# Optimization experiments

Hardware: AMD Instinct MI355X
Metric: run time of the kernel (lower is better)

The kernel has to match this reference:

```python
import jax, jax.numpy as jnp
import numpy as np

NUM_HEADS = 16
D_MODEL = 1024
D_K = D_MODEL // NUM_HEADS
MAX_SEQ_LEN = 4096
ROPE_BASE = 10000.0
BATCH = 2
SEQ_LEN = 2048


def _rope_tables(seq_len, d_k, base=ROPE_BASE):
    # theta_i = 1 / base^(2i/d_k), i = 0..d_k/2-1
    theta = 1.0 / base ** (jnp.arange(0, d_k, 2, dtype=jnp.float32) / d_k)
    m = jnp.arange(seq_len, dtype=jnp.float32)
    m_theta = jnp.outer(m, theta)                      # [S, d_k/2]
    ang = jnp.concatenate([m_theta, m_theta], axis=-1)  # [S, d_k]
    return jnp.cos(ang), jnp.sin(ang)


def _apply_rope(x, cos, sin):
    # x: [B, H, S, d_k]; rotate-half: cat(-x2, x1)
    d2 = x.shape[-1] // 2
    x1, x2 = x[..., :d2], x[..., d2:]
    x_flip = jnp.concatenate([-x2, x1], axis=-1)
    return x * cos + x_flip * sin


def setup_inputs() -> dict:
    key = jax.random.key(0)
    kx, kq, kk, kv, ko = jax.random.split(key, 5)
    s = 1.0 / np.sqrt(D_MODEL)  # ~ nn.Linear default init scale
    x = jax.random.normal(kx, (BATCH, SEQ_LEN, D_MODEL), dtype=jnp.float32)
    W_Q = jax.random.uniform(kq, (D_MODEL, D_MODEL), jnp.float32, -s, s)
    W_K = jax.random.uniform(kk, (D_MODEL, D_MODEL), jnp.float32, -s, s)
    W_V = jax.random.uniform(kv, (D_MODEL, D_MODEL), jnp.float32, -s, s)
    W_O = jax.random.uniform(ko, (D_MODEL, D_MODEL), jnp.float32, -s, s)
    return {"x": x, "W_Q": W_Q, "W_K": W_K, "W_V": W_V, "W_O": W_O}


def reference(x, W_Q, W_K, W_V, W_O):
    B, S, _ = x.shape
    # Linear with weight [out, in]: y = x @ W.T
    def proj(W):
        y = jnp.einsum('bsd,ed->bse', x, W)
        return y.reshape(B, S, NUM_HEADS, D_K).transpose(0, 2, 1, 3)  # [B,H,S,dk]
    Q, K, V = proj(W_Q), proj(W_K), proj(W_V)
    cos, sin = _rope_tables(S, D_K)
    Q = _apply_rope(Q, cos, sin)
    K = _apply_rope(K, cos, sin)
    scores = jnp.einsum('bhsd,bhtd->bhst', Q, K) / jnp.sqrt(jnp.float32(D_K))
    causal = jnp.tril(jnp.ones((S, S), dtype=bool))
    scores = jnp.where(causal[None, None], scores, -jnp.inf)
    attn = jax.nn.softmax(scores, axis=-1)
    out = jnp.einsum('bhst,bhtd->bhsd', attn, V)
    out = out.transpose(0, 2, 1, 3).reshape(B, S, D_MODEL)
    return jnp.einsum('bsd,ed->bse', out, W_O)
```

## Files before the change

kernel.cpp:

```cpp
#include <hip/hip_runtime.h>
#include <hip/hip_bf16.h>

#define BATCH 2
#define SEQ 2048
#define DM 1024
#define NH 16
#define DKH 64

typedef __attribute__((ext_vector_type(8))) __bf16 bf16x8;
typedef __attribute__((ext_vector_type(4))) float f32x4;
typedef __attribute__((ext_vector_type(2))) float f32x2;
typedef __attribute__((ext_vector_type(8))) unsigned short ushort8;

__device__ __forceinline__ void gload16(const void* g, void* l) {
  __builtin_amdgcn_global_load_lds(
      (const __attribute__((address_space(1))) void*)g,
      (__attribute__((address_space(3))) void*)l, 16, 0, 0);
}

__global__ void cast_x(const float* __restrict__ in, __bf16* __restrict__ out) {
  int i = blockIdx.x * blockDim.x + threadIdx.x;
  f32x4 a = ((const f32x4*)in)[2 * i], b = ((const f32x4*)in)[2 * i + 1];
  bf16x8 o;
  o[0]=(__bf16)a[0]; o[1]=(__bf16)a[1]; o[2]=(__bf16)a[2]; o[3]=(__bf16)a[3];
  o[4]=(__bf16)b[0]; o[5]=(__bf16)b[1]; o[6]=(__bf16)b[2]; o[7]=(__bf16)b[3];
  ((bf16x8*)out)[i] = o;
}

__global__ void cast_w(const float* __restrict__ w0, const float* __restrict__ w1,
                       const float* __restrict__ w2, const float* __restrict__ w3,
                       __bf16* __restrict__ out) {
  const float* src = (blockIdx.y == 0) ? w0 : (blockIdx.y == 1) ? w1
                   : (blockIdx.y == 2) ? w2 : w3;
  __bf16* dst = out + (size_t)blockIdx.y * (DM * DM);
  int i = blockIdx.x * blockDim.x + threadIdx.x;
  f32x4 a = ((const f32x4*)src)[2 * i], b = ((const f32x4*)src)[2 * i + 1];
  bf16x8 o;
  o[0]=(__bf16)a[0]; o[1]=(__bf16)a[1]; o[2]=(__bf16)a[2]; o[3]=(__bf16)a[3];
  o[4]=(__bf16)b[0]; o[5]=(__bf16)b[1]; o[6]=(__bf16)b[2]; o[7]=(__bf16)b[3];
  ((bf16x8*)dst)[i] = o;
}

__global__ void gen_tab(float* __restrict__ tab) {
  int idx = blockIdx.x * blockDim.x + threadIdx.x;
  int s = idx >> 5, i = idx & 31;
  float theta = exp2f((float)i * -0.41524101186092029f);
  float sn, c;
  sincosf((float)s * theta, &sn, &c);
  tab[2 * idx] = c;
  tab[2 * idx + 1] = sn;
}

#define QSCALE 0.1803368801111137f

template<int EPI, int BN>
__launch_bounds__(256, 3)
__global__ void gemm_bt(const __bf16* __restrict__ A, const __bf16* __restrict__ B,
                        void* __restrict__ Cout, int M, int N, int K,
                        const float* __restrict__ tab) {
  __shared__ __bf16 As[128 * 64];
  __shared__ __bf16 Bs[BN * 64];
  const int tid = threadIdx.x;
  const int lane = tid & 63;
  const int w = tid >> 6;
  const int wr = w >> 1, wc = w & 1;
  const int fr = lane & 15, fq = lane >> 4;
  const int lid = blockIdx.y * gridDim.x + blockIdx.x;
  const int total = gridDim.x * gridDim.y;
  const int nlid = (lid >> 3) + (lid & 7) * (total >> 3);
  const int bx = nlid & 31;
  const int by = nlid >> 5;
  const int m0 = bx * 128;
  const int n0 = by * BN;
  const int NFR = BN / 32;

  f32x4 acc[4][BN / 32] = {};
  const int NT = K >> 6;

  for (int kt = 0; kt < NT; ++kt) {
    const int k0 = kt << 6;
    __syncthreads();
    #pragma unroll
    for (int p = 0; p < 4; ++p) {
      int c = p * 256 + tid;
      int row = c >> 3, cs = (c & 7) ^ (row & 7);
      gload16(&A[(size_t)(m0 + row) * K + k0 + cs * 8], &As[(p * 256 + w * 64) * 8]);
    }
    #pragma unroll
    for (int p = 0; p < BN / 32; ++p) {
      int c = p * 256 + tid;
      int row = c >> 3, cs = (c & 7) ^ (row & 7);
      gload16(&B[(size_t)(n0 + row) * K + k0 + cs * 8], &Bs[(p * 256 + w * 64) * 8]);
    }
    __syncthreads();
    #pragma unroll
    for (int kk = 0; kk < 2; ++kk) {
      bf16x8 af[4], bfr[BN / 32];
      #pragma unroll
      for (int mf = 0; mf < 4; ++mf) {
        int row = wr * 64 + mf * 16 + fr;
        af[mf] = *(const bf16x8*)&As[row * 64 + ((kk * 32 + fq * 8) ^ ((fr & 7) << 3))];
      }
      #pragma unroll
      for (int nf = 0; nf < NFR; ++nf) {
        int row = wc * (BN / 2) + nf * 16 + fr;
        bfr[nf] = *(const bf16x8*)&Bs[row * 64 + ((kk * 32 + fq * 8) ^ ((fr & 7) << 3))];
      }
      __builtin_amdgcn_s_setprio(1);
      #pragma unroll
      for (int mf = 0; mf < 4; ++mf)
        #pragma unroll
        for (int nf = 0; nf < NFR; ++nf)
          acc[mf][nf] = __builtin_amdgcn_mfma_f32_16x16x32_bf16(af[mf], bfr[nf], acc[mf][nf], 0, 0, 0);
      __builtin_amdgcn_s_setprio(0);
    }
  }

  if (EPI == 0) {
    const int nbase = n0 + wc * 64;
    const int which = nbase >> 10;
    const int h = (nbase & 1023) >> 6;
    const int b = m0 >> 11;
    __bf16* base0 = (__bf16*)Cout + (size_t)which * (4u << 20);
    if (which < 2) {
      const float scale = (which == 0) ? QSCALE : 1.0f;
      __bf16* dst = base0 + ((size_t)(b * NH + h)) * SEQ * DKH;
      #pragma unroll
      for (int mf = 0; mf < 4; ++mf) {
        #pragma unroll
        for (int j = 0; j < 4; ++j) {
          int s = (m0 & (SEQ - 1)) + wr * 64 + mf * 16 + fq * 4 + j;
          #pragma unroll
          for (int nf = 0; nf < 2; ++nf) {
            int i = nf * 16 + fr;
            f32x2 cs = ((const f32x2*)tab)[s * 32 + i];
            float a = acc[mf][nf][j], bb = acc[mf][nf + 2][j];
            dst[(size_t)s * DKH + i]      = (__bf16)((a * cs[0] - bb * cs[1]) * scale);
            dst[(size_t)s * DKH + i + 32] = (__bf16)((bb * cs[0] + a * cs[1]) * scale);
          }
        }
      }
    } else {
      __bf16* dst = base0 + ((size_t)(b * NH + h)) * DKH * SEQ;
      #pragma unroll
      for (int mf = 0; mf < 4; ++mf) {
        #pragma unroll
        for (int nf = 0; nf < 4; ++nf) {
          int dk = nf * 16 + fr;
          #pragma unroll
          for (int j = 0; j < 4; ++j) {
            int sp = (m0 & (SEQ - 1)) + wr * 64 + (mf >> 1) * 32 + fq * 8 + (mf & 1) * 4 + j;
            dst[(size_t)dk * SEQ + sp] = (__bf16)acc[mf][nf][j];
          }
        }
      }
    }
  } else {
    #pragma unroll
    for (int mf = 0; mf < 4; ++mf)
      #pragma unroll
      for (int nf = 0; nf < NFR; ++nf)
        #pragma unroll
        for (int j = 0; j < 4; ++j) {
          int m = m0 + wr * 64 + mf * 16 + fq * 4 + j;
          int n = n0 + wc * (BN / 2) + nf * 16 + fr;
          ((float*)Cout)[(size_t)m * N + n] = acc[mf][nf][j];
        }
  }
}

__launch_bounds__(512, 4)
__global__ void attn_causal(const __bf16* __restrict__ Qg, const __bf16* __restrict__ Kg,
                            const __bf16* __restrict__ Vtg, __bf16* __restrict__ Out,
                            float* __restrict__ P0, float* __restrict__ P1,
                            float* __restrict__ L0, float* __restrict__ L1) {
  __shared__ __bf16 Ks[2][64 * 64];
  __shared__ __bf16 Vts[2][64 * 64];
  const int tid = threadIdx.x;
  const int lane = tid & 63;
  const int w = tid >> 6;
  const int fr = lane & 15, fq = lane >> 4;
  const int bid = blockIdx.x;
  const int bh = bid >> 4;
  const int slot = bid & 15;
  const bool isA = slot < 8;
  const int qa = slot;
  const int qb = isA ? (15 - slot) : slot;
  const int sw  = isA ? (2 * qa + 2) : 99;
  const int off = isA ? (15 - 2 * qa) : 0;
  const int b = bh >> 4, h = bh & 15;
  const __bf16* Qh = Qg + (size_t)bh * SEQ * DKH;
  const __bf16* Kh = Kg + (size_t)bh * SEQ * DKH;
  const __bf16* Vth = Vtg + (size_t)bh * DKH * SEQ;

  int qrow_lo = (isA ? qa : qb) * 128 + w * 16;

  bf16x8 qf[2];
  #pragma unroll
  for (int kk = 0; kk < 2; ++kk)
    qf[kk] = *(const bf16x8*)&Qh[(size_t)(qrow_lo + fr) * DKH + kk * 32 + fq * 8];

  f32x4 Oa[4] = {};
  float lsum = 0.f;

  {
    int cch = w * 64 + lane;
    int row = cch >> 3, cs = (cch & 7) ^ (row & 7);
    gload16(&Kh[(size_t)row * DKH + cs * 8], &Ks[0][(w * 64) * 8]);
    gload16(&Vth[(size_t)row * SEQ + cs * 8], &Vts[0][(w * 64) * 8]);
  }
  __syncthreads();

  for (int it = 0; it < 17; ++it) {
    const int cur = it & 1;
    if (it + 1 < 17) {
      const int nx = it + 1;
      const int kvn = (nx < sw) ? nx : nx + off;
      const int tn = kvn << 6;
      int cch = w * 64 + lane;
      int row = cch >> 3, cs = (cch & 7) ^ (row & 7);
      gload16(&Kh[(size_t)(tn + row) * DKH + cs * 8], &Ks[cur ^ 1][(w * 64) * 8]);
      gload16(&Vth[(size_t)row * SEQ + tn + cs * 8], &Vts[cur ^ 1][(w * 64) * 8]);
    }
    if (isA && it == sw) {
      float ls = lsum;
      ls += __shfl_xor(ls, 16);
      ls += __shfl_xor(ls, 32);
      float rl[4];
      #pragma unroll
      for (int j = 0; j < 4; ++j)
        rl[j] = 1.0f / __shfl(ls, fq * 4 + j);
      #pragma unroll
      for (int nf = 0; nf < 4; ++nf)
        #pragma unroll
        for (int j = 0; j < 4; ++j) {
          int qr = qrow_lo + fq * 4 + j;
          Out[((size_t)(b * SEQ) + qr) * DM + h * DKH + nf * 16 + fr] =
              (__bf16)(Oa[nf][j] * rl[j]);
        }
      #pragma unroll
      for (int nf = 0; nf < 4; ++nf) Oa[nf] = (f32x4){0.f, 0.f, 0.f, 0.f};
      lsum = 0.f;
      qrow_lo = qb * 128 + w * 16;
      #pragma unroll
      for (int kk = 0; kk < 2; ++kk)
        qf[kk] = *(const bf16x8*)&Qh[(size_t)(qrow_lo + fr) * DKH + kk * 32 + fq * 8];
    }
    const int kvt = (it < sw) ? it : it + off;
    const int ts = kvt << 6;
    if (ts <= qrow_lo + 15) {
      f32x4 sacc[4] = {};
      __builtin_amdgcn_s_setprio(1);
      #pragma unroll
      for (int kk = 0; kk < 2; ++kk) {
        #pragma unroll
        for (int nf = 0; nf < 4; ++nf) {
          int krow = nf * 16 + fr;
          bf16x8 kf = *(const bf16x8*)&Ks[cur][krow * 64 + ((kk * 32 + fq * 8) ^ ((fr & 7) << 3))];
          sacc[nf] = __builtin_amdgcn_mfma_f32_16x16x32_bf16(kf, qf[kk], sacc[nf], 0, 0, 0);
        }
      }
      __builtin_amdgcn_s_setprio(0);
      const bool need_mask = (ts + 63 > qrow_lo);
      if (need_mask) {
        const int qr = qrow_lo + fr;
        #pragma unroll
        for (int nf = 0; nf < 4; ++nf) {
          #pragma unroll
          for (int j = 0; j < 4; ++j) {
            float v = sacc[nf][j];
            int tc = ts + nf * 16 + fq * 4 + j;
            if (tc > qr) v = -INFINITY;
            float pv = exp2f(v);
            lsum += pv;
            sacc[nf][j] = pv;
          }
        }
      } else {
        #pragma unroll
        for (int nf = 0; nf < 4; ++nf) {
          #pragma unroll
          for (int j = 0; j < 4; ++j) {
            float pv = exp2f(sacc[nf][j]);
            lsum += pv;
            sacc[nf][j] = pv;
          }
        }
      }
      bf16x8 pa[2];
      #pragma unroll
      for (int kk = 0; kk < 2; ++kk)
        #pragma unroll
        for (int e = 0; e < 8; ++e)
          pa[kk][e] = (__bf16)sacc[2 * kk + (e >> 2)][e & 3];
      __builtin_amdgcn_s_setprio(1);
      #pragma unroll
      for (int kk = 0; kk < 2; ++kk) {
        #pragma unroll
        for (int nf = 0; nf < 4; ++nf) {
          int d = nf * 16 + fr;
          bf16x8 vf = *(const bf16x8*)&Vts[cur][d * 64 + ((kk * 32 + fq * 8) ^ ((fr & 7) << 3))];
          Oa[nf] = __builtin_amdgcn_mfma_f32_16x16x32_bf16(pa[kk], vf, Oa[nf], 0, 0, 0);
        }
      }
      __builtin_amdgcn_s_setprio(0);
    }
    __syncthreads();
  }
  float* P = isA ? P1 : P0;
  float* L = isA ? L1 : L0;
  const int rbase = ((bh << 3) + (qb - 8)) << 7;
  float ls = lsum;
  ls += __shfl_xor(ls, 16);
  ls += __shfl_xor(ls, 32);
  if (lane < 16) L[rbase + w * 16 + lane] = ls;
  #pragma unroll
  for (int nf = 0; nf < 4; ++nf)
    #pragma unroll
    for (int j = 0; j < 4; ++j)
      P[(size_t)(rbase + w * 16 + fq * 4 + j) * 64 + nf * 16 + fr] = Oa[nf][j];
}

__global__ void combine(const float* __restrict__ P0, const float* __restrict__ P1,
                        const float* __restrict__ L0, const float* __restrict__ L1,
                        __bf16* __restrict__ Ab) {
  int t = blockIdx.x * blockDim.x + threadIdx.x;
  int rowid = t >> 3, d0 = (t & 7) * 8;
  int bh = rowid >> 10, rem = rowid & 1023;
  int tq = rem >> 7, r = rem & 127;
  float rl = 1.0f / (L0[rowid] + L1[rowid]);
  const float* p0 = P0 + (size_t)rowid * 64 + d0;
  const float* p1 = P1 + (size_t)rowid * 64 + d0;
  f32x4 a0 = *(const f32x4*)p0, a1 = *(const f32x4*)(p0 + 4);
  f32x4 b0 = *(const f32x4*)p1, b1 = *(const f32x4*)(p1 + 4);
  bf16x8 o;
  #pragma unroll
  for (int e = 0; e < 4; ++e) {
    o[e]     = (__bf16)((a0[e] + b0[e]) * rl);
    o[e + 4] = (__bf16)((a1[e] + b1[e]) * rl);
  }
  int s = (tq + 8) * 128 + r;
  int b = bh >> 4, h = bh & 15;
  *(bf16x8*)&Ab[((size_t)b * SEQ + s) * DM + h * DKH + d0] = o;
}

extern "C" void kernel_launch(void* const* d_in, const int* in_sizes, int n_in,
                              void* d_out, int out_size, void* d_ws, size_t ws_size,
                              hipStream_t stream) {
  const float* x  = (const float*)d_in[0];
  const float* Wq = (const float*)d_in[1];
  const float* Wk = (const float*)d_in[2];
  const float* Wv = (const float*)d_in[3];
  const float* Wo = (const float*)d_in[4];

  char* ws = (char*)d_ws;
  __bf16* xb  = (__bf16*)(ws);
  __bf16* wqb = (__bf16*)(ws + ( 8u << 20));
  __bf16* wob = (__bf16*)(ws + (14u << 20));
  __bf16* Qb  = (__bf16*)(ws + (16u << 20));
  __bf16* Kb  = (__bf16*)(ws + (24u << 20));
  __bf16* Vtb = (__bf16*)(ws + (32u << 20));
  __bf16* Ab  = (__bf16*)(ws + (40u << 20));
  float*  tab = (float*)(ws + (48u << 20));
  float*  L0  = (float*)(ws + (49u << 20));
  float*  L1  = (float*)(ws + (49u << 20) + (1u << 18));
  float* P0 = (float*)d_out;
  float* P1 = P0 + (32768 * 64);

  cast_x<<<dim3(2048), dim3(256), 0, stream>>>(x, xb);
  cast_w<<<dim3(512, 4), dim3(256), 0, stream>>>(Wq, Wk, Wv, Wo, wqb);
  gen_tab<<<dim3(256), dim3(256), 0, stream>>>(tab);

  gemm_bt<0, 128><<<dim3(32, 24), dim3(256), 0, stream>>>(xb, wqb, Qb, BATCH * SEQ, 3 * DM, DM, tab);

  attn_causal<<<dim3(512), dim3(512), 0, stream>>>(Qb, Kb, Vtb, Ab, P0, P1, L0, L1);

  combine<<<dim3(1024), dim3(256), 0, stream>>>(P0, P1, L0, L1, Ab);

  gemm_bt<1, 64><<<dim3(32, 16), dim3(256), 0, stream>>>(Ab, wob, d_out, BATCH * SEQ, DM, DM, nullptr);
}
```

Measured before the change: 104.3 us.

## Triple-buffer K/V tiles in causal attention with deeper async prefetch

Extends the K/V shared-memory ring from two to three buffers and prefetches two tiles ahead via global_load_lds. The end-of-iteration __syncthreads is replaced by an explicit vmcnt wait plus a single barrier at the start of each iteration. This is meant to hide global load latency and remove one barrier per iteration. The cost is more LDS per block, which may reduce resident blocks per CU.

```diff
diff --git a/kernel.cpp b/kernel.cpp
--- a/kernel.cpp
+++ b/kernel.cpp
@@ -174,8 +174,8 @@
                             const __bf16* __restrict__ Vtg, __bf16* __restrict__ Out,
                             float* __restrict__ P0, float* __restrict__ P1,
                             float* __restrict__ L0, float* __restrict__ L1) {
-  __shared__ __bf16 Ks[2][64 * 64];
-  __shared__ __bf16 Vts[2][64 * 64];
+  __shared__ __bf16 Ks[3][64 * 64];
+  __shared__ __bf16 Vts[3][64 * 64];
   const int tid = threadIdx.x;
   const int lane = tid & 63;
   const int w = tid >> 6;
@@ -195,6 +195,16 @@
 
   int qrow_lo = (isA ? qa : qb) * 128 + w * 16;
 
+  const int cch = w * 64 + lane;
+  const int srow = cch >> 3;
+  const int scs = ((cch & 7) ^ (srow & 7)) * 8;
+
+#define STAGE(buf, kvt) {                                                     \
+    gload16(&Kh[(size_t)(((kvt) << 6) + srow) * DKH + scs],                   \
+            &Ks[buf][(w * 64) * 8]);                                          \
+    gload16(&Vth[(size_t)srow * SEQ + ((kvt) << 6) + scs],                    \
+            &Vts[buf][(w * 64) * 8]); }
+
   bf16x8 qf[2];
   #pragma unroll
   for (int kk = 0; kk < 2; ++kk)
@@ -203,24 +213,19 @@
   f32x4 Oa[4] = {};
   float lsum = 0.f;
 
-  {
-    int cch = w * 64 + lane;
-    int row = cch >> 3, cs = (cch & 7) ^ (row & 7);
-    gload16(&Kh[(size_t)row * DKH + cs * 8], &Ks[0][(w * 64) * 8]);
-    gload16(&Vth[(size_t)row * SEQ + cs * 8], &Vts[0][(w * 64) * 8]);
-  }
-  __syncthreads();
+  STAGE(0, 0);
+  STAGE(1, 1);
 
   for (int it = 0; it < 17; ++it) {
-    const int cur = it & 1;
-    if (it + 1 < 17) {
-      const int nx = it + 1;
+    const int cur = it % 3;
+    if (it < 16) asm volatile("s_waitcnt vmcnt(2)" ::: "memory");
+    else         asm volatile("s_waitcnt vmcnt(0)" ::: "memory");
+    __builtin_amdgcn_s_barrier();
+    if (it + 2 < 17) {
+      const int nx = it + 2;
       const int kvn = (nx < sw) ? nx : nx + off;
-      const int tn = kvn << 6;
-      int cch = w * 64 + lane;
-      int row = cch >> 3, cs = (cch & 7) ^ (row & 7);
-      gload16(&Kh[(size_t)(tn + row) * DKH + cs * 8], &Ks[cur ^ 1][(w * 64) * 8]);
-      gload16(&Vth[(size_t)row * SEQ + tn + cs * 8], &Vts[cur ^ 1][(w * 64) * 8]);
+      const int nb = (it + 2) % 3;
+      STAGE(nb, kvn);
     }
     if (isA && it == sw) {
       float ls = lsum;
@@ -305,8 +310,8 @@
       }
       __builtin_amdgcn_s_setprio(0);
     }
-    __syncthreads();
   }
+#undef STAGE
   float* P = isA ? P1 : P0;
   float* L = isA ? L1 : L0;
   const int rbase = ((bh << 3) + (qb - 8)) << 7;
```

After: 103.7 us. Within noise of the previous version (-0.6%).

## Stage 128-row KV tiles per barrier and remap block order in causal attention

Applied to the files above, without the earlier changes.

The attention kernel now loads K and V^T tiles of 128 keys per double-buffer stage instead of 64. Each stage is processed as two 64-key sub-tiles, which cuts the loop from 17 iterations with barriers to at most 9. Block IDs are also remapped so that consecutive blocks are spread across head/slot groups, likely to improve load balance or cache locality across XCDs. The cost is twice the LDS per block (64KB), which may reduce occupancy under the 512x4 launch bounds, plus some wasted loads for partially masked tiles.

```diff
diff --git a/kernel.cpp b/kernel.cpp
--- a/kernel.cpp
+++ b/kernel.cpp
@@ -174,20 +174,22 @@
                             const __bf16* __restrict__ Vtg, __bf16* __restrict__ Out,
                             float* __restrict__ P0, float* __restrict__ P1,
                             float* __restrict__ L0, float* __restrict__ L1) {
-  __shared__ __bf16 Ks[2][64 * 64];
-  __shared__ __bf16 Vts[2][64 * 64];
+  __shared__ __bf16 Ks[2][128 * 64];
+  __shared__ __bf16 Vts[2][64 * 128];
   const int tid = threadIdx.x;
   const int lane = tid & 63;
   const int w = tid >> 6;
   const int fr = lane & 15, fq = lane >> 4;
-  const int bid = blockIdx.x;
-  const int bh = bid >> 4;
-  const int slot = bid & 15;
+  const int r = blockIdx.x;
+  const int nlid = (r & 7) * 64 + (r >> 3);
+  const int bh = nlid >> 4;
+  const int slot = nlid & 15;
   const bool isA = slot < 8;
   const int qa = slot;
   const int qb = isA ? (15 - slot) : slot;
-  const int sw  = isA ? (2 * qa + 2) : 99;
-  const int off = isA ? (15 - 2 * qa) : 0;
+  const int sw  = isA ? (qa + 1) : 99;
+  const int off = isA ? (8 - qa) : 0;
+  const int nst = isA ? 8 : 9;
   const int b = bh >> 4, h = bh & 15;
   const __bf16* Qh = Qg + (size_t)bh * SEQ * DKH;
   const __bf16* Kh = Kg + (size_t)bh * SEQ * DKH;
@@ -195,6 +197,19 @@
 
   int qrow_lo = (isA ? qa : qb) * 128 + w * 16;
 
+  const int ck0 = tid, ck1 = 512 + tid;
+  const int kr0 = ck0 >> 3, kc0 = ((ck0 & 7) ^ (kr0 & 7)) * 8;
+  const int kr1 = ck1 >> 3, kc1 = ((ck1 & 7) ^ (kr1 & 7)) * 8;
+  const int vd0 = ck0 >> 4, vk0 = (((ck0 & 15) & 8) | (((ck0 & 15) ^ vd0) & 7)) * 8;
+  const int vd1 = ck1 >> 4, vk1 = (((ck1 & 15) & 8) | (((ck1 & 15) ^ vd1) & 7)) * 8;
+
+#define STAGE(buf, kvt) {                                                     \
+    const int ts_ = (kvt) << 7;                                               \
+    gload16(&Kh[(size_t)(ts_ + kr0) * DKH + kc0], &Ks[buf][(w * 64) * 8]);    \
+    gload16(&Kh[(size_t)(ts_ + kr1) * DKH + kc1], &Ks[buf][(512 + w * 64) * 8]); \
+    gload16(&Vth[(size_t)vd0 * SEQ + ts_ + vk0], &Vts[buf][(w * 64) * 8]);    \
+    gload16(&Vth[(size_t)vd1 * SEQ + ts_ + vk1], &Vts[buf][(512 + w * 64) * 8]); }
+
   bf16x8 qf[2];
   #pragma unroll
   for (int kk = 0; kk < 2; ++kk)
@@ -203,24 +218,15 @@
   f32x4 Oa[4] = {};
   float lsum = 0.f;
 
-  {
-    int cch = w * 64 + lane;
-    int row = cch >> 3, cs = (cch & 7) ^ (row & 7);
-    gload16(&Kh[(size_t)row * DKH + cs * 8], &Ks[0][(w * 64) * 8]);
-    gload16(&Vth[(size_t)row * SEQ + cs * 8], &Vts[0][(w * 64) * 8]);
-  }
+  STAGE(0, 0);
   __syncthreads();
 
-  for (int it = 0; it < 17; ++it) {
+  for (int it = 0; it < 9; ++it) {
     const int cur = it & 1;
-    if (it + 1 < 17) {
+    if (it + 1 < nst) {
       const int nx = it + 1;
       const int kvn = (nx < sw) ? nx : nx + off;
-      const int tn = kvn << 6;
-      int cch = w * 64 + lane;
-      int row = cch >> 3, cs = (cch & 7) ^ (row & 7);
-      gload16(&Kh[(size_t)(tn + row) * DKH + cs * 8], &Ks[cur ^ 1][(w * 64) * 8]);
-      gload16(&Vth[(size_t)row * SEQ + tn + cs * 8], &Vts[cur ^ 1][(w * 64) * 8]);
+      STAGE(cur ^ 1, kvn);
     }
     if (isA && it == sw) {
       float ls = lsum;
@@ -246,67 +252,73 @@
       for (int kk = 0; kk < 2; ++kk)
         qf[kk] = *(const bf16x8*)&Qh[(size_t)(qrow_lo + fr) * DKH + kk * 32 + fq * 8];
     }
-    const int kvt = (it < sw) ? it : it + off;
-    const int ts = kvt << 6;
-    if (ts <= qrow_lo + 15) {
-      f32x4 sacc[4] = {};
-      __builtin_amdgcn_s_setprio(1);
-      #pragma unroll
-      for (int kk = 0; kk < 2; ++kk) {
-        #pragma unroll
-        for (int nf = 0; nf < 4; ++nf) {
-          int krow = nf * 16 + fr;
-          bf16x8 kf = *(const bf16x8*)&Ks[cur][krow * 64 + ((kk * 32 + fq * 8) ^ ((fr & 7) << 3))];
-          sacc[nf] = __builtin_amdgcn_mfma_f32_16x16x32_bf16(kf, qf[kk], sacc[nf], 0, 0, 0);
-        }
-      }
-      __builtin_amdgcn_s_setprio(0);
-      const bool need_mask = (ts + 63 > qrow_lo);
-      if (need_mask) {
-        const int qr = qrow_lo + fr;
-        #pragma unroll
-        for (int nf = 0; nf < 4; ++nf) {
-          #pragma unroll
-          for (int j = 0; j < 4; ++j) {
-            float v = sacc[nf][j];
-            int tc = ts + nf * 16 + fq * 4 + j;
-            if (tc > qr) v = -INFINITY;
-            float pv = exp2f(v);
-            lsum += pv;
-            sacc[nf][j] = pv;
-          }
-        }
-      } else {
-        #pragma unroll
-        for (int nf = 0; nf < 4; ++nf) {
-          #pragma unroll
-          for (int j = 0; j < 4; ++j) {
-            float pv = exp2f(sacc[nf][j]);
-            lsum += pv;
-            sacc[nf][j] = pv;
-          }
-        }
-      }
-      bf16x8 pa[2];
-      #pragma unroll
-      for (int kk = 0; kk < 2; ++kk)
-        #pragma unroll
-        for (int e = 0; e < 8; ++e)
-          pa[kk][e] = (__bf16)sacc[2 * kk + (e >> 2)][e & 3];
-      __builtin_amdgcn_s_setprio(1);
-      #pragma unroll
-      for (int kk = 0; kk < 2; ++kk) {
-        #pragma unroll
-        for (int nf = 0; nf < 4; ++nf) {
-          int d = nf * 16 + fr;
-          bf16x8 vf = *(const bf16x8*)&Vts[cur][d * 64 + ((kk * 32 + fq * 8) ^ ((fr & 7) << 3))];
-          Oa[nf] = __builtin_amdgcn_mfma_f32_16x16x32_bf16(pa[kk], vf, Oa[nf], 0, 0, 0);
-        }
-      }
-      __builtin_amdgcn_s_setprio(0);
+    if (it < nst) {
+      const int kvt = (it < sw) ? it : it + off;
+      #pragma unroll
+      for (int sub = 0; sub < 2; ++sub) {
+        const int ts = (kvt << 7) + (sub << 6);
+        if (ts > qrow_lo + 15) continue;
+        f32x4 sacc[4] = {};
+        __builtin_amdgcn_s_setprio(1);
+        #pragma unroll
+        for (int kk = 0; kk < 2; ++kk) {
+          #pragma unroll
+          for (int nf = 0; nf < 4; ++nf) {
+            int krow = (sub << 6) + nf * 16 + fr;
+            bf16x8 kf = *(const bf16x8*)&Ks[cur][krow * 64 + ((kk * 32 + fq * 8) ^ ((fr & 7) << 3))];
+            sacc[nf] = __builtin_amdgcn_mfma_f32_16x16x32_bf16(kf, qf[kk], sacc[nf], 0, 0, 0);
+          }
+        }
+        __builtin_amdgcn_s_setprio(0);
+        const bool need_mask = (ts + 63 > qrow_lo);
+        if (need_mask) {
+          const int qr = qrow_lo + fr;
+          #pragma unroll
+          for (int nf = 0; nf < 4; ++nf) {
+            #pragma unroll
+            for (int j = 0; j < 4; ++j) {
+              float v = sacc[nf][j];
+              int tc = ts + nf * 16 + fq * 4 + j;
+              if (tc > qr) v = -INFINITY;
+              float pv = exp2f(v);
+              lsum += pv;
+              sacc[nf][j] = pv;
+            }
+          }
+        } else {
+          #pragma unroll
+          for (int nf = 0; nf < 4; ++nf) {
+            #pragma unroll
+            for (int j = 0; j < 4; ++j) {
+              float pv = exp2f(sacc[nf][j]);
+              lsum += pv;
+              sacc[nf][j] = pv;
+            }
+          }
+        }
+        bf16x8 pa[2];
+        #pragma unroll
+        for (int kk = 0; kk < 2; ++kk)
+          #pragma unroll
+          for (int e = 0; e < 8; ++e)
+            pa[kk][e] = (__bf16)sacc[2 * kk + (e >> 2)][e & 3];
+        __builtin_amdgcn_s_setprio(1);
+        #pragma unroll
+        for (int kk = 0; kk < 2; ++kk) {
+          #pragma unroll
+          for (int nf = 0; nf < 4; ++nf) {
+            int d = nf * 16 + fr;
+            bf16x8 vf = *(const bf16x8*)&Vts[cur][d * 128 + (sub << 6) +
+                         (((kk * 4 + fq) ^ (fr & 7)) << 3)];
+            Oa[nf] = __builtin_amdgcn_mfma_f32_16x16x32_bf16(pa[kk], vf, Oa[nf], 0, 0, 0);
+          }
+        }
+        __builtin_amdgcn_s_setprio(0);
+      }
     }
     __syncthreads();
   }
+#undef STAGE
   float* P = isA ? P1 : P0;
   float* L = isA ? L1 : L0;
   const int rbase = ((bh << 3) + (qb - 8)) << 7;
```

Result: faster. 101.2 us (-2.9%).

## Split causal attention into 64-row query tiles with 256-thread blocks and XCD-aware ordering

Applied to the files above, without the earlier changes.

Attention blocks now handle 64-row query tiles with 4 waves instead of 128-row tiles with 8 waves, and the grid doubles to 1024 blocks. Each block pairs a low and a high query tile for load balance, and block IDs are remapped so that consecutive heads are spread across the 8 XCDs. K/V staging now loads two chunks per thread, and the partial-output indexing and combine kernel are updated for the new tiling. The aim is more blocks, better occupancy and better L2 locality, at the cost of more redundant K/V loads per query row.

```diff
diff --git a/kernel.cpp b/kernel.cpp
--- a/kernel.cpp
+++ b/kernel.cpp
@@ -169,7 +169,7 @@
   }
 }
 
-__launch_bounds__(512, 4)
+__launch_bounds__(256, 4)
 __global__ void attn_causal(const __bf16* __restrict__ Qg, const __bf16* __restrict__ Kg,
                             const __bf16* __restrict__ Vtg, __bf16* __restrict__ Out,
                             float* __restrict__ P0, float* __restrict__ P1,
@@ -180,20 +180,34 @@
   const int lane = tid & 63;
   const int w = tid >> 6;
   const int fr = lane & 15, fq = lane >> 4;
-  const int bid = blockIdx.x;
-  const int bh = bid >> 4;
-  const int slot = bid & 15;
-  const bool isA = slot < 8;
+  const int r = blockIdx.x;
+  const int nlid = (r & 7) * 128 + (r >> 3);
+  const int bh = nlid >> 5;
+  const int slot = nlid & 31;
+  const bool isA = slot < 16;
   const int qa = slot;
-  const int qb = isA ? (15 - slot) : slot;
-  const int sw  = isA ? (2 * qa + 2) : 99;
-  const int off = isA ? (15 - 2 * qa) : 0;
+  const int qb = isA ? (31 - slot) : slot;
+  const int sw  = isA ? (qa + 1) : 99;
+  const int off = isA ? (16 - qa) : 0;
+  const int nst = isA ? 16 : 17;
   const int b = bh >> 4, h = bh & 15;
   const __bf16* Qh = Qg + (size_t)bh * SEQ * DKH;
   const __bf16* Kh = Kg + (size_t)bh * SEQ * DKH;
   const __bf16* Vth = Vtg + (size_t)bh * DKH * SEQ;
 
-  int qrow_lo = (isA ? qa : qb) * 128 + w * 16;
+  int qrow_lo = (isA ? qa : qb) * 64 + w * 16;
+
+#define STAGE(buf, kvt) {                                                     \
+    const int ts_ = (kvt) << 6;                                               \
+    _Pragma("unroll")                                                         \
+    for (int p = 0; p < 2; ++p) {                                             \
+      int c = p * 256 + tid;                                                  \
+      int row = c >> 3, cs = (c & 7) ^ (row & 7);                             \
+      gload16(&Kh[(size_t)(ts_ + row) * DKH + cs * 8],                        \
+              &Ks[buf][(p * 256 + w * 64) * 8]);                              \
+      gload16(&Vth[(size_t)row * SEQ + ts_ + cs * 8],                         \
+              &Vts[buf][(p * 256 + w * 64) * 8]);                             \
+    } }
 
   bf16x8 qf[2];
   #pragma unroll
@@ -203,24 +217,15 @@
   f32x4 Oa[4] = {};
   float lsum = 0.f;
 
-  {
-    int cch = w * 64 + lane;
-    int row = cch >> 3, cs = (cch & 7) ^ (row & 7);
-    gload16(&Kh[(size_t)row * DKH + cs * 8], &Ks[0][(w * 64) * 8]);
-    gload16(&Vth[(size_t)row * SEQ + cs * 8], &Vts[0][(w * 64) * 8]);
-  }
+  STAGE(0, 0);
   __syncthreads();
 
   for (int it = 0; it < 17; ++it) {
     const int cur = it & 1;
-    if (it + 1 < 17) {
+    if (it + 1 < nst) {
       const int nx = it + 1;
       const int kvn = (nx < sw) ? nx : nx + off;
-      const int tn = kvn << 6;
-      int cch = w * 64 + lane;
-      int row = cch >> 3, cs = (cch & 7) ^ (row & 7);
-      gload16(&Kh[(size_t)(tn + row) * DKH + cs * 8], &Ks[cur ^ 1][(w * 64) * 8]);
-      gload16(&Vth[(size_t)row * SEQ + tn + cs * 8], &Vts[cur ^ 1][(w * 64) * 8]);
+      STAGE(cur ^ 1, kvn);
     }
     if (isA && it == sw) {
       float ls = lsum;
@@ -241,84 +246,87 @@
       #pragma unroll
       for (int nf = 0; nf < 4; ++nf) Oa[nf] = (f32x4){0.f, 0.f, 0.f, 0.f};
       lsum = 0.f;
-      qrow_lo = qb * 128 + w * 16;
+      qrow_lo = qb * 64 + w * 16;
       #pragma unroll
       for (int kk = 0; kk < 2; ++kk)
         qf[kk] = *(const bf16x8*)&Qh[(size_t)(qrow_lo + fr) * DKH + kk * 32 + fq * 8];
     }
-    const int kvt = (it < sw) ? it : it + off;
-    const int ts = kvt << 6;
-    if (ts <= qrow_lo + 15) {
-      f32x4 sacc[4] = {};
-      __builtin_amdgcn_s_setprio(1);
-      #pragma unroll
-      for (int kk = 0; kk < 2; ++kk) {
-        #pragma unroll
-        for (int nf = 0; nf < 4; ++nf) {
-          int krow = nf * 16 + fr;
-          bf16x8 kf = *(const bf16x8*)&Ks[cur][krow * 64 + ((kk * 32 + fq * 8) ^ ((fr & 7) << 3))];
-          sacc[nf] = __builtin_amdgcn_mfma_f32_16x16x32_bf16(kf, qf[kk], sacc[nf], 0, 0, 0);
-        }
-      }
-      __builtin_amdgcn_s_setprio(0);
-      const bool need_mask = (ts + 63 > qrow_lo);
-      if (need_mask) {
-        const int qr = qrow_lo + fr;
-        #pragma unroll
-        for (int nf = 0; nf < 4; ++nf) {
-          #pragma unroll
-          for (int j = 0; j < 4; ++j) {
-            float v = sacc[nf][j];
-            int tc = ts + nf * 16 + fq * 4 + j;
-            if (tc > qr) v = -INFINITY;
-            float pv = exp2f(v);
-            lsum += pv;
-            sacc[nf][j] = pv;
-          }
-        }
-      } else {
-        #pragma unroll
-        for (int nf = 0; nf < 4; ++nf) {
-          #pragma unroll
-          for (int j = 0; j < 4; ++j) {
-            float pv = exp2f(sacc[nf][j]);
-            lsum += pv;
-            sacc[nf][j] = pv;
-          }
-        }
-      }
-      bf16x8 pa[2];
-      #pragma unroll
-      for (int kk = 0; kk < 2; ++kk)
-        #pragma unroll
-        for (int e = 0; e < 8; ++e)
-          pa[kk][e] = (__bf16)sacc[2 * kk + (e >> 2)][e & 3];
-      __builtin_amdgcn_s_setprio(1);
-      #pragma unroll
-      for (int kk = 0; kk < 2; ++kk) {
-        #pragma unroll
-        for (int nf = 0; nf < 4; ++nf) {
-          int d = nf * 16 + fr;
-          bf16x8 vf = *(const bf16x8*)&Vts[cur][d * 64 + ((kk * 32 + fq * 8) ^ ((fr & 7) << 3))];
-          Oa[nf] = __builtin_amdgcn_mfma_f32_16x16x32_bf16(pa[kk], vf, Oa[nf], 0, 0, 0);
-        }
-      }
-      __builtin_amdgcn_s_setprio(0);
+    if (it < nst) {
+      const int kvt = (it < sw) ? it : it + off;
+      const int ts = kvt << 6;
+      if (ts <= qrow_lo + 15) {
+        f32x4 sacc[4] = {};
+        __builtin_amdgcn_s_setprio(1);
+        #pragma unroll
+        for (int kk = 0; kk < 2; ++kk) {
+          #pragma unroll
+          for (int nf = 0; nf < 4; ++nf) {
+            int krow = nf * 16 + fr;
+            bf16x8 kf = *(const bf16x8*)&Ks[cur][krow * 64 + ((kk * 32 + fq * 8) ^ ((fr & 7) << 3))];
+            sacc[nf] = __builtin_amdgcn_mfma_f32_16x16x32_bf16(kf, qf[kk], sacc[nf], 0, 0, 0);
+          }
+        }
+        __builtin_amdgcn_s_setprio(0);
+        const bool need_mask = (ts + 63 > qrow_lo);
+        if (need_mask) {
+          const int qr = qrow_lo + fr;
+          #pragma unroll
+          for (int nf = 0; nf < 4; ++nf) {
+            #pragma unroll
+            for (int j = 0; j < 4; ++j) {
+              float v = sacc[nf][j];
+              int tc = ts + nf * 16 + fq * 4 + j;
+              if (tc > qr) v = -INFINITY;
+              float pv = exp2f(v);
+              lsum += pv;
+              sacc[nf][j] = pv;
+            }
+          }
+        } else {
+          #pragma unroll
+          for (int nf = 0; nf < 4; ++nf) {
+            #pragma unroll
+            for (int j = 0; j < 4; ++j) {
+              float pv = exp2f(sacc[nf][j]);
+              lsum += pv;
+              sacc[nf][j] = pv;
+            }
+          }
+        }
+        bf16x8 pa[2];
+        #pragma unroll
+        for (int kk = 0; kk < 2; ++kk)
+          #pragma unroll
+          for (int e = 0; e < 8; ++e)
+            pa[kk][e] = (__bf16)sacc[2 * kk + (e >> 2)][e & 3];
+        __builtin_amdgcn_s_setprio(1);
+        #pragma unroll
+        for (int kk = 0; kk < 2; ++kk) {
+          #pragma unroll
+          for (int nf = 0; nf < 4; ++nf) {
+            int d = nf * 16 + fr;
+            bf16x8 vf = *(const bf16x8*)&Vts[cur][d * 64 + ((kk * 32 + fq * 8) ^ ((fr & 7) << 3))];
+            Oa[nf] = __builtin_amdgcn_mfma_f32_16x16x32_bf16(pa[kk], vf, Oa[nf], 0, 0, 0);
+          }
+        }
+        __builtin_amdgcn_s_setprio(0);
+      }
     }
     __syncthreads();
   }
+#undef STAGE
   float* P = isA ? P1 : P0;
   float* L = isA ? L1 : L0;
-  const int rbase = ((bh << 3) + (qb - 8)) << 7;
+  const int rbase = (bh << 10) + ((qb - 16) << 6) + w * 16;
   float ls = lsum;
   ls += __shfl_xor(ls, 16);
   ls += __shfl_xor(ls, 32);
-  if (lane < 16) L[rbase + w * 16 + lane] = ls;
+  if (lane < 16) L[rbase + lane] = ls;
   #pragma unroll
   for (int nf = 0; nf < 4; ++nf)
     #pragma unroll
     for (int j = 0; j < 4; ++j)
-      P[(size_t)(rbase + w * 16 + fq * 4 + j) * 64 + nf * 16 + fr] = Oa[nf][j];
+      P[(size_t)(rbase + fq * 4 + j) * 64 + nf * 16 + fr] = Oa[nf][j];
 }
 
 __global__ void combine(const float* __restrict__ P0, const float* __restrict__ P1,
@@ -327,7 +335,6 @@
   int t = blockIdx.x * blockDim.x + threadIdx.x;
   int rowid = t >> 3, d0 = (t & 7) * 8;
   int bh = rowid >> 10, rem = rowid & 1023;
-  int tq = rem >> 7, r = rem & 127;
   float rl = 1.0f / (L0[rowid] + L1[rowid]);
   const float* p0 = P0 + (size_t)rowid * 64 + d0;
   const float* p1 = P1 + (size_t)rowid * 64 + d0;
@@ -339,7 +346,7 @@
     o[e]     = (__bf16)((a0[e] + b0[e]) * rl);
     o[e + 4] = (__bf16)((a1[e] + b1[e]) * rl);
   }
-  int s = (tq + 8) * 128 + r;
+  int s = 1024 + rem;
   int b = bh >> 4, h = bh & 15;
   *(bf16x8*)&Ab[((size_t)b * SEQ + s) * DM + h * DKH + d0] = o;
 }
@@ -373,7 +380,7 @@
 
   gemm_bt<0, 128><<<dim3(32, 24), dim3(256), 0, stream>>>(xb, wqb, Qb, BATCH * SEQ, 3 * DM, DM, tab);
 
-  attn_causal<<<dim3(512), dim3(512), 0, stream>>>(Qb, Kb, Vtb, Ab, P0, P1, L0, L1);
+  attn_causal<<<dim3(1024), dim3(256), 0, stream>>>(Qb, Kb, Vtb, Ab, P0, P1, L0, L1);
 
   combine<<<dim3(1024), dim3(256), 0, stream>>>(P0, P1, L0, L1, Ab);
 
```

After: 103.8 us. Within noise of the previous version (-0.5%).
